# Kernel tuning notes

Measured on AMD Instinct MI355X. Metric: run time of the kernel, lower is better.

Reference implementation:

```python
import jax, jax.numpy as jnp
import numpy as np

jax.config.update("jax_enable_x64", True)

B = 16384          # batch size (rows of features)
K = 256            # num_unlabel (clusters)
EPS = 0.05         # sinkhorn epsilon
GAMMA = 5.0        # KL regularizer weight
LR = 0.1           # SGD lr for w
MOM = 0.99         # SGD momentum
N_INNER = 3        # sinkhorn iterations
N_OUTER = 10       # outer optimization iterations


def setup_inputs() -> dict:
    key = jax.random.key(0)
    features = jax.random.normal(key, (B, K), dtype=jnp.float32)
    w = jnp.ones((1, K), dtype=jnp.float32) / K  # torch Parameter init: ones/K
    return {"features": features, "w": w, "head": 0}


def _sinkhorn(logits, w):
    """SinkhornKnopp_im.forward: logits [B,K] -> Q [B,K] (float64), preds=logits64."""
    logits64 = logits.astype(jnp.float64)
    Q = jnp.exp(logits64 / EPS).T            # [K, B]
    Q = Q / jnp.sum(Q)
    K2 = jax.nn.softmax(w, axis=1).astype(jnp.float64)  # [1, K] marginal prior
    Bn = Q.shape[1]
    for _ in range(N_INNER):
        Q = Q / jnp.sum(Q, axis=1, keepdims=True)       # row normalize
        Q = Q * K2.T                                    # scale rows by prior
        Q = Q / jnp.sum(Q, axis=0, keepdims=True)       # column normalize
        Q = Q / Bn
    Q = Q * Bn
    return Q.T, logits64                                # [B, K], [B, K]


def _total_loss(w, features):
    Q, preds = _sinkhorn(features, w)
    loss = -jnp.mean(jnp.sum(Q * preds, axis=1))
    # KLDivLoss(batchmean): input = log_softmax(w).T [K,1], target = softmax(w0).T = 1/K
    logw = jax.nn.log_softmax(w, axis=1)[0]             # [K]
    t = jnp.float32(1.0 / K)
    reg = jnp.sum(t * (jnp.log(t) - logw)) / K
    return loss + GAMMA * reg.astype(jnp.float64), Q


def reference(features, w, head):
    features = jax.lax.stop_gradient(features)  # features.detach()

    def step(carry, _):
        w, buf, _ = carry
        (_, Q), g = jax.value_and_grad(_total_loss, has_aux=True)(w, features)
        # clip_grad_norm_(params, 1)
        norm = jnp.sqrt(jnp.sum(g.astype(jnp.float64) ** 2)).astype(g.dtype)
        g = g * jnp.minimum(jnp.float32(1.0), jnp.float32(1.0) / (norm + 1e-6))
        # SGD with momentum 0.99 (buf starts at 0 -> first buf = g, matching torch)
        buf = MOM * buf + g
        w = w - LR * buf
        return (w, buf, Q), None

    Q0 = jnp.zeros((features.shape[0], K), dtype=jnp.float64)
    (w_f, buf_f, Q), _ = jax.lax.scan(
        step, (w, jnp.zeros_like(w), Q0), None, length=N_OUTER
    )
    return Q  # Q from the last outer iteration (computed with pre-update w)
```

## Files before the change

kernel.cpp:

```cpp
#include <hip/hip_runtime.h>


namespace {

constexpr int KDIM = 256;
constexpr int NBLK = 256;
constexpr int ROWS = 64;
constexpr int NREP = 16;
constexpr int NPH  = 48;
constexpr float L2E20 = 28.853900817779268f;

constexpr size_t P_DBL   = 2ull * NBLK * KDIM;
constexpr size_t RES_OFF = P_DBL;
constexpr size_t RES_DBL = (size_t)NPH * NREP * KDIM;
constexpr size_t WS_DBL  = P_DBL + RES_DBL;

__device__ __forceinline__ double fast_exp_d(double x) {
  const double LOG2E  = 1.4426950408889634074;
  const double LN2_HI = 6.93147180369123816490e-01;
  const double LN2_LO = 1.90821492927058770002e-10;
  double n = rint(x * LOG2E);
  double t = fma(-n, LN2_HI, x);
  t = fma(-n, LN2_LO, t);
  double p = 2.4801587301587302e-05;
  p = fma(p, t, 1.9841269841269841e-04);
  p = fma(p, t, 1.3888888888888889e-03);
  p = fma(p, t, 8.3333333333333333e-03);
  p = fma(p, t, 4.1666666666666664e-02);
  p = fma(p, t, 1.6666666666666666e-01);
  p = fma(p, t, 0.5);
  p = fma(p, t, 1.0);
  p = fma(p, t, 1.0);
  long long ni = (long long)n;
  double s = __longlong_as_double((unsigned long long)(ni + 1023LL) << 52);
  return p * s;
}

__device__ __forceinline__ double wave_sum_d(double v) {
#pragma unroll
  for (int o = 32; o > 0; o >>= 1) v += __shfl_down(v, o);
  return v;
}
__device__ __forceinline__ double wave_max_d(double v) {
#pragma unroll
  for (int o = 32; o > 0; o >>= 1) v = fmax(v, __shfl_down(v, o));
  return v;
}

__device__ __forceinline__ double pload(const double* p) {
  return __hip_atomic_load(p, __ATOMIC_RELAXED, __HIP_MEMORY_SCOPE_AGENT);
}
__device__ __forceinline__ void pstore(double* p, double v) {
  __hip_atomic_store(p, v, __ATOMIC_RELAXED, __HIP_MEMORY_SCOPE_AGENT);
}

}

__global__ __launch_bounds__(256) void kInitWS(double* __restrict__ ws) {
  const double QN = __builtin_nan("");
  size_t gid = (size_t)blockIdx.x * 256 + threadIdx.x;
  size_t stride = (size_t)gridDim.x * 256;
  for (size_t j = gid; j < WS_DBL; j += stride) ws[j] = QN;
}

__global__ __launch_bounds__(256, 1) void sink_main(
    const float* __restrict__ feat, const float* __restrict__ w_in,
    float* __restrict__ out, double* __restrict__ ws) {
  __shared__ float  Et[ROWS * KDIM];
  __shared__ float  Ft[ROWS * KDIM];
  __shared__ double alpha[KDIM];
  __shared__ double v1s[ROWS], v2s[ROWS], v3s[ROWS];
  __shared__ double grow[ROWS], wrow[ROWS], sbr[ROWS];
  __shared__ float  mrow[ROWS];
  __shared__ double sred[8];

  const int t = threadIdx.x, bid = blockIdx.x;
  const int wv = t >> 6, lane = t & 63;
  const int b0 = bid * ROWS;
  const double QN = __builtin_nan("");

  double* P   = ws;
  double* res = ws + RES_OFF;

  auto blk_sum = [&](double v) -> double {
    v = wave_sum_d(v);
    __syncthreads();
    if (lane == 0) sred[wv] = v;
    __syncthreads();
    return sred[0] + sred[1] + sred[2] + sred[3];
  };
  auto blk_max = [&](double v) -> double {
    v = wave_max_d(v);
    __syncthreads();
    if (lane == 0) sred[wv + 4] = v;
    __syncthreads();
    return fmax(fmax(sred[4], sred[5]), fmax(sred[6], sred[7]));
  };

  auto allreduce = [&](unsigned ph, double pa) -> double {
    const int p = ph & 1;
    pstore(P + ((size_t)p * NBLK + bid) * KDIM + t, pa);
    double* e = P + ((size_t)p * NBLK + t) * KDIM + bid;
    double v;
    for (;;) {
      v = pload(e);
      if (!__builtin_isnan(v)) break;
      __builtin_amdgcn_s_sleep(1);
    }
    pstore(e, QN);
    v = wave_sum_d(v);
    __syncthreads();
    if (lane == 0) sred[wv] = v;
    __syncthreads();
    double s = sred[0] + sred[1] + sred[2] + sred[3];
    if (t < NREP) pstore(res + ((size_t)ph * NREP + t) * KDIM + bid, s);
    const double* re = res + ((size_t)ph * NREP + (bid & (NREP - 1))) * KDIM + t;
    double r;
    for (;;) {
      r = pload(re);
      if (!__builtin_isnan(r)) break;
      __builtin_amdgcn_s_sleep(1);
    }
    return r;
  };

  auto row_pass = [&](double* dstv) {
    double a0 = alpha[4 * lane + 0], a1 = alpha[4 * lane + 1];
    double a2 = alpha[4 * lane + 2], a3 = alpha[4 * lane + 3];
#pragma unroll 4
    for (int r = wv; r < ROWS; r += 4) {
      float4 e4 = ((const float4*)(Et + r * KDIM))[lane];
      double s1 = a0 * (double)e4.x + a1 * (double)e4.y +
                  a2 * (double)e4.z + a3 * (double)e4.w;
      s1 = wave_sum_d(s1);
      if (lane == 0) dstv[r] = s1;
    }
  };
  auto col_partial = [&]() -> double {
    double a = 0.0;
#pragma unroll 8
    for (int r = 0; r < ROWS; ++r) a += (double)Et[r * KDIM + t] * wrow[r];
    return a;
  };

  {
    const float4* src = (const float4*)(feat + (size_t)b0 * KDIM);
    float4* dst = (float4*)Ft;
#pragma unroll
    for (int s = 0; s < 16; ++s) dst[s * 256 + t] = src[s * 256 + t];
  }
  __syncthreads();
  for (int r = wv; r < ROWS; r += 4) {
    float4 f4 = ((const float4*)(Ft + r * KDIM))[lane];
    float m = fmaxf(fmaxf(f4.x, f4.y), fmaxf(f4.z, f4.w));
#pragma unroll
    for (int o = 32; o > 0; o >>= 1) m = fmaxf(m, __shfl_down(m, o));
    if (lane == 0) {
      mrow[r] = m;
      sbr[r] = fast_exp_d(20.0 * (double)m);
    }
  }
  __syncthreads();
  double pu0 = 0.0;
#pragma unroll 8
  for (int r = 0; r < ROWS; ++r) {
    float e = exp2f((Ft[r * KDIM + t] - mrow[r]) * L2E20);
    Et[r * KDIM + t] = e;
    pu0 += (double)e * sbr[r];
  }
  float w_t = w_in[t], buf_t = 0.0f;
  double k2_t;
  {
    double x = (double)w_t;
    double m = blk_max(x);
    double e = fast_exp_d(x - m);
    double s = blk_sum(e);
    k2_t = e / s;
  }
  unsigned ph = 0;
  double u0_t = allreduce(ph, pu0);

  for (int it = 0; it < 10; ++it) {
    double u1_t, u2_t;

    alpha[t] = k2_t / u0_t;
    __syncthreads();
    row_pass(v1s);
    __syncthreads();
    if (t < ROWS) wrow[t] = 1.0 / (16384.0 * v1s[t]);
    __syncthreads();
    {
      double pa = col_partial();
      ++ph; u1_t = allreduce(ph, pa);
    }

    alpha[t] = k2_t / u1_t;
    __syncthreads();
    row_pass(v2s);
    __syncthreads();
    if (t < ROWS) wrow[t] = 1.0 / (16384.0 * v2s[t]);
    __syncthreads();
    {
      double pa = col_partial();
      ++ph; u2_t = allreduce(ph, pa);
    }

    if (it == 9) {
      alpha[t] = k2_t / u2_t;
      __syncthreads();
      row_pass(v3s);
      __syncthreads();
      if (t < ROWS) wrow[t] = 1.0 / v3s[t];
      __syncthreads();
      double a3 = alpha[t];
#pragma unroll 4
      for (int r = 0; r < ROWS; ++r)
        out[(size_t)(b0 + r) * KDIM + t] =
            (float)(a3 * (double)Et[r * KDIM + t] * wrow[r]);
      return;
    }

    alpha[t] = k2_t / u2_t;
    __syncthreads();
    {
      double a0 = alpha[4 * lane + 0], a1 = alpha[4 * lane + 1];
      double a2 = alpha[4 * lane + 2], a3 = alpha[4 * lane + 3];
#pragma unroll 2
      for (int r = wv; r < ROWS; r += 4) {
        float4 e4 = ((const float4*)(Et + r * KDIM))[lane];
        float4 f4 = ((const float4*)(Ft + r * KDIM))[lane];
        double p0 = a0 * (double)e4.x, p1 = a1 * (double)e4.y;
        double p2 = a2 * (double)e4.z, p3 = a3 * (double)e4.w;
        double s1 = p0 + p1 + p2 + p3;
        double s2 = p0 * (double)f4.x + p1 * (double)f4.y +
                    p2 * (double)f4.z + p3 * (double)f4.w;
        s1 = wave_sum_d(s1);
        s2 = wave_sum_d(s2);
        if (lane == 0) {
          v3s[r] = s1;
          grow[r] = s2 / (16384.0 * s1 * s1);
        }
      }
    }
    __syncthreads();
    if (t < ROWS) wrow[t] = -1.0 / (16384.0 * v3s[t]);
    __syncthreads();
    double gsum_t;
    {
      double ac1 = 0.0, ac2 = 0.0;
#pragma unroll 8
      for (int r = 0; r < ROWS; ++r) {
        double ed = (double)Et[r * KDIM + t];
        ac1 += ed * (double)Ft[r * KDIM + t] * wrow[r];
        ac2 += ed * grow[r];
      }
      ++ph; gsum_t = allreduce(ph, ac1 + ac2);
    }

    alpha[t] = -gsum_t * k2_t / (u2_t * u2_t);
    __syncthreads();
    row_pass(grow);
    __syncthreads();
    if (t < ROWS) wrow[t] = -grow[t] / (16384.0 * v2s[t] * v2s[t]);
    __syncthreads();
    double ga2_t;
    {
      double pa = col_partial();
      ++ph; ga2_t = allreduce(ph, pa);
    }

    alpha[t] = -ga2_t * k2_t / (u1_t * u1_t);
    __syncthreads();
    row_pass(grow);
    __syncthreads();
    if (t < ROWS) wrow[t] = -grow[t] / (16384.0 * v1s[t] * v1s[t]);
    __syncthreads();
    double ga1_t;
    {
      double pa = col_partial();
      ++ph; ga1_t = allreduce(ph, pa);
    }

    {
      double gk2 = gsum_t / u2_t + ga2_t / u1_t + ga1_t / u0_t;
      double dot = blk_sum(k2_t * gk2);
      double gw = k2_t * (gk2 - dot) + 5.0 * (k2_t / 256.0 - 1.0 / 65536.0);
      double n2 = blk_sum(gw * gw);
      float normf = (float)sqrt(n2);
      float sc = fminf(1.0f, 1.0f / (normf + 1e-6f));
      float g = (float)gw * sc;
      buf_t = 0.99f * buf_t + g;
      w_t = w_t - 0.1f * buf_t;
      double x = (double)w_t;
      double m = blk_max(x);
      double e = fast_exp_d(x - m);
      double s = blk_sum(e);
      k2_t = e / s;
    }
  }
}

extern "C" void kernel_launch(void* const* d_in, const int* in_sizes, int n_in,
                              void* d_out, int out_size, void* d_ws,
                              size_t ws_size, hipStream_t stream) {
  (void)in_sizes; (void)n_in; (void)out_size; (void)ws_size;
  const float* feat = (const float*)d_in[0];
  const float* w_in = (const float*)d_in[1];
  float* out = (float*)d_out;
  double* ws = (double*)d_ws;

  kInitWS<<<128, 256, 0, stream>>>(ws);
  sink_main<<<NBLK, 256, 0, stream>>>(feat, w_in, out, ws);
}
```

Measured before the change: 659.4 us.

## Replace NaN-sentinel all-to-all allreduce with two-level grouped flag-based reduction

Replaces the cross-block allreduce, which used a transposed all-to-all exchange with NaN sentinels and replicated result broadcast, with a two-level tree. Blocks are split into 8 groups of 32. Non-leader blocks write their partial vector and a phase-tagged flag, and the group leader sums the 31 partials and publishes a group sum. Every block then waits on the 8 group flags and sums the 8 group vectors. This cuts the per-phase polling and traffic fan-in and drops the NaN reset stores, but puts a serial leader step on the critical path and adds explicit memory-ordering waits.

```diff
diff --git a/kernel.cpp b/kernel.cpp
--- a/kernel.cpp
+++ b/kernel.cpp
@@ -6,14 +6,15 @@
 constexpr int KDIM = 256;
 constexpr int NBLK = 256;
 constexpr int ROWS = 64;
-constexpr int NREP = 16;
-constexpr int NPH  = 48;
+constexpr int NGRP = 8;
+constexpr int GSZ  = 32;
 constexpr float L2E20 = 28.853900817779268f;
 
-constexpr size_t P_DBL   = 2ull * NBLK * KDIM;
-constexpr size_t RES_OFF = P_DBL;
-constexpr size_t RES_DBL = (size_t)NPH * NREP * KDIM;
-constexpr size_t WS_DBL  = P_DBL + RES_DBL;
+constexpr size_t S1V_OFF = 0;
+constexpr size_t S1T_OFF = 131072;
+constexpr size_t S2V_OFF = 131584;
+constexpr size_t S2T_OFF = 135680;
+constexpr size_t WS_DBL  = 135808;
 
 __device__ __forceinline__ double fast_exp_d(double x) {
   const double LOG2E  = 1.4426950408889634074;
@@ -77,10 +78,12 @@
   const int t = threadIdx.x, bid = blockIdx.x;
   const int wv = t >> 6, lane = t & 63;
   const int b0 = bid * ROWS;
-  const double QN = __builtin_nan("");
-
-  double* P   = ws;
-  double* res = ws + RES_OFF;
+  const int grp = bid >> 5, rank = bid & 31;
+
+  double* S1V = ws + S1V_OFF;
+  double* S1T = ws + S1T_OFF;
+  double* S2V = ws + S2V_OFF;
+  double* S2T = ws + S2T_OFF;
 
   auto blk_sum = [&](double v) -> double {
     v = wave_sum_d(v);
@@ -98,30 +101,58 @@
   };
 
   auto allreduce = [&](unsigned ph, double pa) -> double {
-    const int p = ph & 1;
-    pstore(P + ((size_t)p * NBLK + bid) * KDIM + t, pa);
-    double* e = P + ((size_t)p * NBLK + t) * KDIM + bid;
-    double v;
-    for (;;) {
-      v = pload(e);
-      if (!__builtin_isnan(v)) break;
-      __builtin_amdgcn_s_sleep(1);
-    }
-    pstore(e, QN);
-    v = wave_sum_d(v);
-    __syncthreads();
-    if (lane == 0) sred[wv] = v;
-    __syncthreads();
-    double s = sred[0] + sred[1] + sred[2] + sred[3];
-    if (t < NREP) pstore(res + ((size_t)ph * NREP + t) * KDIM + bid, s);
-    const double* re = res + ((size_t)ph * NREP + (bid & (NREP - 1))) * KDIM + t;
-    double r;
-    for (;;) {
-      r = pload(re);
-      if (!__builtin_isnan(r)) break;
-      __builtin_amdgcn_s_sleep(1);
-    }
-    return r;
+    const int par = (int)(ph & 1);
+    const double dph = (double)ph;
+    if (rank == 0) {
+      if (t >= 1 && t < GSZ) {
+        const double* tp = S1T + ((size_t)par * NGRP + grp) * GSZ + t;
+        while (pload(tp) != dph) __builtin_amdgcn_s_sleep(1);
+      }
+      __syncthreads();
+      double acc = pa;
+      {
+        const double* B = S1V + (((size_t)par * NGRP + grp) * GSZ) * KDIM + t;
+#pragma unroll
+        for (int g = 0; g < 3; ++g) {
+          const double* r0 = B + (size_t)(1 + 8 * g) * KDIM;
+          double w0 = pload(r0 + 0 * KDIM), w1 = pload(r0 + 1 * KDIM);
+          double w2 = pload(r0 + 2 * KDIM), w3 = pload(r0 + 3 * KDIM);
+          double w4 = pload(r0 + 4 * KDIM), w5 = pload(r0 + 5 * KDIM);
+          double w6 = pload(r0 + 6 * KDIM), w7 = pload(r0 + 7 * KDIM);
+          acc += w0; acc += w1; acc += w2; acc += w3;
+          acc += w4; acc += w5; acc += w6; acc += w7;
+        }
+        const double* r0 = B + (size_t)25 * KDIM;
+        double w0 = pload(r0 + 0 * KDIM), w1 = pload(r0 + 1 * KDIM);
+        double w2 = pload(r0 + 2 * KDIM), w3 = pload(r0 + 3 * KDIM);
+        double w4 = pload(r0 + 4 * KDIM), w5 = pload(r0 + 5 * KDIM);
+        double w6 = pload(r0 + 6 * KDIM);
+        acc += w0; acc += w1; acc += w2; acc += w3;
+        acc += w4; acc += w5; acc += w6;
+      }
+      pstore(S2V + ((size_t)par * NGRP + grp) * KDIM + t, acc);
+      asm volatile("s_waitcnt vmcnt(0)" ::: "memory");
+      __syncthreads();
+      if (t == 0) pstore(S2T + ((size_t)par * NGRP + grp) * 8, dph);
+    } else {
+      pstore(S1V + (((size_t)par * NGRP + grp) * GSZ + rank) * KDIM + t, pa);
+      asm volatile("s_waitcnt vmcnt(0)" ::: "memory");
+      __syncthreads();
+      if (t == 0) pstore(S1T + ((size_t)par * NGRP + grp) * GSZ + rank, dph);
+    }
+    if (t < NGRP) {
+      const double* sp = S2T + ((size_t)par * NGRP + t) * 8;
+      while (pload(sp) != dph) __builtin_amdgcn_s_sleep(1);
+    }
+    __syncthreads();
+    const double* V = S2V + (size_t)par * NGRP * KDIM + t;
+    double x0 = pload(V + 0 * KDIM), x1 = pload(V + 1 * KDIM);
+    double x2 = pload(V + 2 * KDIM), x3 = pload(V + 3 * KDIM);
+    double x4 = pload(V + 4 * KDIM), x5 = pload(V + 5 * KDIM);
+    double x6 = pload(V + 6 * KDIM), x7 = pload(V + 7 * KDIM);
+    double tot = x0;
+    tot += x1; tot += x2; tot += x3; tot += x4; tot += x5; tot += x6; tot += x7;
+    return tot;
   };
 
   auto row_pass = [&](double* dstv) {
```

After: 611.7 us. 1.08x faster.

## Replace transpose-style grid allreduce with two-level group reduction

Applied to the files above, without the earlier changes.

The cross-block allreduce is restructured. Before, every block wrote a 256-wide partial, read a transposed column, reduced it in-block and published replicated results. Now blocks form 16 groups of 16: group leaders poll and sum their members' partials, publish a per-group sum, and every block polls all 16 group sums and adds them locally. This drops the in-block shuffle/sync reduction and the replicated result writes, but serialises work through the leaders and has every block poll 16 locations.

```diff
diff --git a/kernel.cpp b/kernel.cpp
--- a/kernel.cpp
+++ b/kernel.cpp
@@ -6,14 +6,12 @@
 constexpr int KDIM = 256;
 constexpr int NBLK = 256;
 constexpr int ROWS = 64;
-constexpr int NREP = 16;
-constexpr int NPH  = 48;
+constexpr int NGRP = 16;
+constexpr int GSZ  = 16;
 constexpr float L2E20 = 28.853900817779268f;
 
-constexpr size_t P_DBL   = 2ull * NBLK * KDIM;
-constexpr size_t RES_OFF = P_DBL;
-constexpr size_t RES_DBL = (size_t)NPH * NREP * KDIM;
-constexpr size_t WS_DBL  = P_DBL + RES_DBL;
+constexpr size_t G2_OFF = 2ull * NGRP * GSZ * KDIM;
+constexpr size_t WS_DBL = G2_OFF + 48ull * NGRP * KDIM;
 
 __device__ __forceinline__ double fast_exp_d(double x) {
   const double LOG2E  = 1.4426950408889634074;
@@ -77,10 +75,8 @@
   const int t = threadIdx.x, bid = blockIdx.x;
   const int wv = t >> 6, lane = t & 63;
   const int b0 = bid * ROWS;
+  const int grp = bid >> 4, rank = bid & 15;
   const double QN = __builtin_nan("");
-
-  double* P   = ws;
-  double* res = ws + RES_OFF;
 
   auto blk_sum = [&](double v) -> double {
     v = wave_sum_d(v);
@@ -98,30 +94,54 @@
   };
 
   auto allreduce = [&](unsigned ph, double pa) -> double {
-    const int p = ph & 1;
-    pstore(P + ((size_t)p * NBLK + bid) * KDIM + t, pa);
-    double* e = P + ((size_t)p * NBLK + t) * KDIM + bid;
-    double v;
+    const int par = (int)(ph & 1);
+    double* Pg  = ws + (((size_t)par * NGRP + grp) * GSZ) * KDIM;
+    double* G2p = ws + G2_OFF + (size_t)ph * NGRP * KDIM;
+    if (rank == 0) {
+      double v[GSZ - 1];
+#pragma unroll
+      for (int r = 0; r < GSZ - 1; ++r)
+        v[r] = pload(Pg + (size_t)(r + 1) * KDIM + t);
+      for (;;) {
+        bool again = false;
+#pragma unroll
+        for (int r = 0; r < GSZ - 1; ++r)
+          if (__builtin_isnan(v[r])) {
+            v[r] = pload(Pg + (size_t)(r + 1) * KDIM + t);
+            if (__builtin_isnan(v[r])) again = true;
+          }
+        if (!again) break;
+        __builtin_amdgcn_s_sleep(1);
+      }
+      double acc = pa;
+#pragma unroll
+      for (int r = 0; r < GSZ - 1; ++r) acc += v[r];
+#pragma unroll
+      for (int r = 0; r < GSZ - 1; ++r)
+        pstore(Pg + (size_t)(r + 1) * KDIM + t, QN);
+      asm volatile("s_waitcnt vmcnt(0)" ::: "memory");
+      pstore(G2p + (size_t)grp * KDIM + t, acc);
+    } else {
+      pstore(Pg + (size_t)rank * KDIM + t, pa);
+    }
+    double g[NGRP];
+#pragma unroll
+    for (int x = 0; x < NGRP; ++x) g[x] = pload(G2p + (size_t)x * KDIM + t);
     for (;;) {
-      v = pload(e);
-      if (!__builtin_isnan(v)) break;
-      __builtin_amdgcn_s_sleep(1);
-    }
-    pstore(e, QN);
-    v = wave_sum_d(v);
-    __syncthreads();
-    if (lane == 0) sred[wv] = v;
-    __syncthreads();
-    double s = sred[0] + sred[1] + sred[2] + sred[3];
-    if (t < NREP) pstore(res + ((size_t)ph * NREP + t) * KDIM + bid, s);
-    const double* re = res + ((size_t)ph * NREP + (bid & (NREP - 1))) * KDIM + t;
-    double r;
-    for (;;) {
-      r = pload(re);
-      if (!__builtin_isnan(r)) break;
-      __builtin_amdgcn_s_sleep(1);
-    }
-    return r;
+      bool again = false;
+#pragma unroll
+      for (int x = 0; x < NGRP; ++x)
+        if (__builtin_isnan(g[x])) {
+          g[x] = pload(G2p + (size_t)x * KDIM + t);
+          if (__builtin_isnan(g[x])) again = true;
+        }
+      if (!again) break;
+      __builtin_amdgcn_s_sleep(4);
+    }
+    double tot = g[0];
+#pragma unroll
+    for (int x = 1; x < NGRP; ++x) tot += g[x];
+    return tot;
   };
 
   auto row_pass = [&](double* dstv) {
```

After: 853.6 us. 1.29x slower.

## Concentrate cross-block allreduce on 16 reducer blocks with batched polling

Applied to the files above, without the earlier changes.

The grid-wide allreduce is reorganised. Previously each of the 256 blocks reduced one column over all blocks and published it to replicated result slots. Now only 16 reducer blocks each gather 16 columns across all 256 blocks' partials, polling 16 loads at once, then reduce within the block and write the replicated results. Other blocks only wait on the result. The aim is fewer per-block reduction steps and fewer polling round trips, at the cost of serialising more work onto 16 blocks and lengthening the critical path through them.

```diff
diff --git a/kernel.cpp b/kernel.cpp
--- a/kernel.cpp
+++ b/kernel.cpp
@@ -6,14 +6,13 @@
 constexpr int KDIM = 256;
 constexpr int NBLK = 256;
 constexpr int ROWS = 64;
+constexpr int NRED = 16;
 constexpr int NREP = 16;
 constexpr int NPH  = 48;
 constexpr float L2E20 = 28.853900817779268f;
 
-constexpr size_t P_DBL   = 2ull * NBLK * KDIM;
-constexpr size_t RES_OFF = P_DBL;
-constexpr size_t RES_DBL = (size_t)NPH * NREP * KDIM;
-constexpr size_t WS_DBL  = P_DBL + RES_DBL;
+constexpr size_t RES_OFF = 2ull * NBLK * KDIM;
+constexpr size_t WS_DBL  = RES_OFF + (size_t)NPH * NREP * KDIM;
 
 __device__ __forceinline__ double fast_exp_d(double x) {
   const double LOG2E  = 1.4426950408889634074;
@@ -69,6 +68,8 @@
   __shared__ float  Et[ROWS * KDIM];
   __shared__ float  Ft[ROWS * KDIM];
   __shared__ double alpha[KDIM];
+  __shared__ double tmp1[KDIM];
+  __shared__ double sfin[16];
   __shared__ double v1s[ROWS], v2s[ROWS], v3s[ROWS];
   __shared__ double grow[ROWS], wrow[ROWS], sbr[ROWS];
   __shared__ float  mrow[ROWS];
@@ -98,28 +99,50 @@
   };
 
   auto allreduce = [&](unsigned ph, double pa) -> double {
-    const int p = ph & 1;
-    pstore(P + ((size_t)p * NBLK + bid) * KDIM + t, pa);
-    double* e = P + ((size_t)p * NBLK + t) * KDIM + bid;
-    double v;
-    for (;;) {
-      v = pload(e);
-      if (!__builtin_isnan(v)) break;
+    const int par = (int)(ph & 1);
+    double* Pp = P + (size_t)par * NBLK * KDIM;
+    double* R  = res + (size_t)ph * NREP * KDIM;
+    pstore(Pp + (size_t)bid * KDIM + t, pa);
+    if (bid < NRED) {
+      const int kl = t & 15, seg = t >> 4;
+      const int k = bid * 16 + kl;
+      double* base = Pp + (size_t)(seg * 16) * KDIM + k;
+      double v[16];
+#pragma unroll
+      for (int j = 0; j < 16; ++j) v[j] = pload(base + (size_t)j * KDIM);
+      for (;;) {
+        bool again = false;
+#pragma unroll
+        for (int j = 0; j < 16; ++j)
+          if (__builtin_isnan(v[j])) {
+            v[j] = pload(base + (size_t)j * KDIM);
+            if (__builtin_isnan(v[j])) again = true;
+          }
+        if (!again) break;
+        __builtin_amdgcn_s_sleep(1);
+      }
+      double a = 0.0;
+#pragma unroll
+      for (int j = 0; j < 16; ++j) a += v[j];
+#pragma unroll
+      for (int j = 0; j < 16; ++j) pstore(base + (size_t)j * KDIM, QN);
+      asm volatile("s_waitcnt vmcnt(0)" ::: "memory");
+      tmp1[t] = a;
+      __syncthreads();
+      if (t < 16) {
+        double s = 0.0;
+#pragma unroll
+        for (int sg = 0; sg < 16; ++sg) s += tmp1[sg * 16 + t];
+        sfin[t] = s;
+      }
+      __syncthreads();
+      pstore(R + (size_t)seg * KDIM + k, sfin[kl]);
+    }
+    const double* re = R + (size_t)(bid & (NREP - 1)) * KDIM + t;
+    double r = pload(re);
+    while (__builtin_isnan(r)) {
       __builtin_amdgcn_s_sleep(1);
-    }
-    pstore(e, QN);
-    v = wave_sum_d(v);
-    __syncthreads();
-    if (lane == 0) sred[wv] = v;
-    __syncthreads();
-    double s = sred[0] + sred[1] + sred[2] + sred[3];
-    if (t < NREP) pstore(res + ((size_t)ph * NREP + t) * KDIM + bid, s);
-    const double* re = res + ((size_t)ph * NREP + (bid & (NREP - 1))) * KDIM + t;
-    double r;
-    for (;;) {
       r = pload(re);
-      if (!__builtin_isnan(r)) break;
-      __builtin_amdgcn_s_sleep(1);
     }
     return r;
   };
```

Measured after the change: 638.6 us. 3.2% less time.
